# Kernel optimization log

Measured on AMD Instinct MI355X. Metric: run time of the kernel, lower is better.

Reference implementation:

```python
import jax, jax.numpy as jnp
import numpy as np

N_NODES = 50000
N_EDGES = 800000
F_IN = 128          # num_node_features == conv_size
L = 4               # num_conv_layers
LIN = 256
OUT = 10
N_GRAPHS = 64


def setup_inputs() -> dict:
    key = jax.random.key(0)
    ks = jax.random.split(key, 8)
    x = jax.random.normal(ks[0], (N_NODES, F_IN), dtype=jnp.float32)
    edge_index = jax.random.randint(ks[1], (2, N_EDGES), 0, N_NODES, dtype=jnp.int64)
    batch = jnp.sort(jax.random.randint(ks[2], (N_NODES,), 0, N_GRAPHS, dtype=jnp.int64))
    pos = jax.random.normal(ks[3], (N_NODES, 3), dtype=jnp.float32)
    # learned params: 4 GCN layers (all [F_IN,F_IN] since in==out==128), cat-JK head
    Ws = jax.random.normal(ks[4], (L, F_IN, F_IN), dtype=jnp.float32) * 0.05
    bs = jnp.zeros((L, F_IN), dtype=jnp.float32)
    Wlin = jax.random.normal(ks[5], (L * F_IN, LIN), dtype=jnp.float32) * 0.05
    blin = jnp.zeros((LIN,), dtype=jnp.float32)
    Wout = jax.random.normal(ks[6], (LIN, OUT), dtype=jnp.float32) * 0.05
    bout = jnp.zeros((OUT,), dtype=jnp.float32)
    return {"x": x, "edge_index": edge_index, "batch": batch, "pos": pos,
            "Ws": Ws, "bs": bs, "Wlin": Wlin, "blin": blin,
            "Wout": Wout, "bout": bout}


def reference(x, edge_index, batch, pos, Ws, bs, Wlin, blin, Wout, bout):
    N = x.shape[0]
    # GCN normalization with added self-loops (PyG gcn_norm, edge_weight=1)
    loop = jnp.arange(N, dtype=edge_index.dtype)
    src = jnp.concatenate([edge_index[0], loop])
    dst = jnp.concatenate([edge_index[1], loop])
    deg = jax.ops.segment_sum(jnp.ones_like(dst, dtype=x.dtype), dst, num_segments=N)
    dinv = jax.lax.rsqrt(deg)  # deg >= 1 due to self-loops
    norm = (dinv[src] * dinv[dst])[:, None]  # [E+N, 1]

    h = x
    xs = []
    for l in range(L):
        t = h @ Ws[l]                                    # [N, F]
        agg = jax.ops.segment_sum(t[src] * norm, dst, num_segments=N)
        h = jax.nn.relu(agg + bs[l])                     # dropout is identity in eval
        xs.append(h)
    hcat = jnp.concatenate(xs, axis=-1)                  # JK 'cat' -> [N, L*F]
    g = jax.ops.segment_max(hcat, batch, num_segments=N_GRAPHS)  # global_max_pool
    return jax.nn.relu(g @ Wlin + blin) @ Wout + bout    # [N_GRAPHS, OUT]
```

## Files before the change

### kernel.cpp

```cpp
#include <hip/hip_runtime.h>
#include <stdint.h>

#define NN    50000
#define NE    800000
#define FD    128
#define NLAY  4
#define NLIN  256
#define NOUTF 10
#define NGR   64
#define NBKT  196
#define MAXB  8192
#define GEMMB 782
#define POOLB 512

typedef _Float16 half8  __attribute__((ext_vector_type(8)));
typedef _Float16 half4  __attribute__((ext_vector_type(4)));
typedef _Float16 half2t __attribute__((ext_vector_type(2)));
typedef float    f32x4  __attribute__((ext_vector_type(4)));

__device__ __forceinline__ int ld_idx(const void* p, int flag, long i){
    return flag ? (int)((const long long*)p)[i] : ((const int*)p)[i];
}

__global__ __launch_bounds__(256) void pre_k(const unsigned* __restrict__ eidx_u,
                                             const float* __restrict__ Ws,
                                             _Float16* __restrict__ WT,
                                             int* __restrict__ zbase, int zn, int zb,
                                             int* __restrict__ sent,
                                             float* __restrict__ scl,
                                             int* __restrict__ flag){
    __shared__ int any;
    const int b = blockIdx.x, tid = threadIdx.x;
    if (b < 256){
        int idx = b*256 + tid;
        int l = idx >> 14;
        int r = idx & 16383;
        int c = r >> 7, k = r & 127;
        WT[idx] = (_Float16)Ws[(l<<14) + (k<<7) + c];
    } else if (b < 256 + zb){
        int i = (b-256)*256 + tid;
        if (i < zn) zbase[i] = 0;
    } else if (b == 256 + zb){
        if (tid < FD/4) sent[tid] = 0;
        if (tid == 0) scl[NN] = 0.f;
    } else {
        if (tid == 0) any = 0;
        __syncthreads();
        if (eidx_u[2*tid + 1] != 0u) atomicOr(&any, 1);
        __syncthreads();
        if (tid == 0) *flag = (any == 0) ? 1 : 0;
    }
}

__global__ __launch_bounds__(1024) void binB_k(const void* __restrict__ eidx,
                                               const int* __restrict__ flag,
                                               int* __restrict__ bktCur,
                                               unsigned* __restrict__ binned){
    __shared__ int hist[NBKT];
    __shared__ int resv[NBKT];
    __shared__ int cur[NBKT];
    const int tid = threadIdx.x;
    const int f = *flag;
    if (tid < NBKT){ hist[tid] = 0; cur[tid] = 0; }
    __syncthreads();

    int bkt[4]; unsigned pk[4];
    #pragma unroll
    for (int u = 0; u < 4; ++u){
        long e = (long)blockIdx.x*4096 + u*1024 + tid;
        if (e < NE){
            int s = ld_idx(eidx, f, e);
            int d = ld_idx(eidx, f, (long)NE + e);
            bkt[u] = d >> 8;
            pk[u]  = ((unsigned)(d & 255) << 16) | (unsigned)s;
            atomicAdd(&hist[bkt[u]], 1);
        } else bkt[u] = -1;
    }
    __syncthreads();
    if (tid < NBKT && hist[tid] > 0)
        resv[tid] = atomicAdd(&bktCur[tid], hist[tid]);
    __syncthreads();
    #pragma unroll
    for (int u = 0; u < 4; ++u){
        if (bkt[u] >= 0){
            int p = resv[bkt[u]] + atomicAdd(&cur[bkt[u]], 1);
            if ((unsigned)p < MAXB) binned[(long)bkt[u]*MAXB + p] = pk[u];
        }
    }
}

__global__ __launch_bounds__(256) void passC_k(const int* __restrict__ bktCur,
                                               const unsigned* __restrict__ binned,
                                               int* __restrict__ rp, int* __restrict__ re,
                                               float* __restrict__ dinv,
                                               unsigned short* __restrict__ cn,
                                               const void* __restrict__ batv,
                                               const int* __restrict__ flag,
                                               int* __restrict__ gstart){
    __shared__ unsigned staged[MAXB];
    __shared__ int cnt[256];
    __shared__ int sc[256];
    __shared__ int cur[256];
    const int tid = threadIdx.x;
    if (blockIdx.x >= NBKT){
        int i = (blockIdx.x - NBKT)*256 + tid;
        if (i >= NN) return;
        int f = *flag;
        int b = ld_idx(batv, f, i);
        if (i == 0){
            for (int g = 0; g <= b; ++g) gstart[g] = 0;
        } else {
            int p = ld_idx(batv, f, i-1);
            for (int g = p+1; g <= b; ++g) gstart[g] = i;
        }
        if (i == NN-1){
            for (int g = b+1; g <= NGR; ++g) gstart[g] = NN;
        }
        return;
    }
    const int b = blockIdx.x;
    int n = bktCur[b]; if (n > MAXB) n = MAXB;
    const long base = (long)b*MAXB;

    cnt[tid] = 0;
    __syncthreads();
    for (int i = tid; i < n; i += 256){
        unsigned rec = binned[base + i];
        staged[i] = rec;
        atomicAdd(&cnt[rec >> 16], 1);
    }
    __syncthreads();
    int c  = cnt[tid];
    int pc = (c + 15) & ~15;
    sc[tid] = pc;
    __syncthreads();
    for (int off = 1; off < 256; off <<= 1){
        int t = (tid >= off) ? sc[tid - off] : 0;
        __syncthreads();
        if (tid >= off) sc[tid] += t;
        __syncthreads();
    }
    int lo = sc[tid] - pc;
    int v = b*256 + tid;
    if (v < NN){
        rp[v]   = (int)base + lo;
        re[v]   = (int)base + lo + pc;
        dinv[v] = rsqrtf((float)(c + 1));
    }
    cur[tid] = lo;
    __syncthreads();
    for (int i = tid; i < n; i += 256){
        unsigned rec = staged[i];
        int j = rec >> 16;
        int p = atomicAdd(&cur[j], 1);
        cn[base + p] = (unsigned short)(rec & 0xFFFFu);
    }
    __syncthreads();
    for (int i = c; i < pc; ++i)
        cn[base + lo + i] = (unsigned short)NN;
}

template<bool F32IN, bool POOL>
__global__ __launch_bounds__(256) void gemm_k(const void* __restrict__ Av,
                                              const _Float16* __restrict__ WT,
                                              const float* __restrict__ dinv,
                                              unsigned char* __restrict__ T,
                                              float* __restrict__ scl,
                                              const _Float16* __restrict__ h,
                                              const int* __restrict__ gstart,
                                              unsigned* __restrict__ gbuf, int lpool){
    const int tid  = threadIdx.x;
    if (POOL && blockIdx.x >= GEMMB){
        __shared__ float red[4][FD];
        int pid = blockIdx.x - GEMMB;
        int g = pid >> 3, part = pid & 7;
        int lane = tid & 63, w = tid >> 6;
        int s0 = gstart[g], s1 = gstart[g+1];
        int len = s1 - s0;
        int chunk = (len + 7) >> 3;
        int a = s0 + part*chunk;
        int b = min(a + chunk, s1);
        int sub = (b - a + 3) >> 2;
        int aa = a + w*sub;
        int bb = min(aa + sub, b);
        const half2t* h2 = reinterpret_cast<const half2t*>(h);
        float m0 = 0.f, m1 = 0.f;
        for (int i = aa; i < bb; ++i){
            half2t x = h2[(long)i*64 + lane];
            m0 = fmaxf(m0, (float)x[0]);
            m1 = fmaxf(m1, (float)x[1]);
        }
        red[w][2*lane]   = m0;
        red[w][2*lane+1] = m1;
        __syncthreads();
        if (w == 0){
            float r0 = fmaxf(fmaxf(red[0][2*lane],   red[1][2*lane]),
                             fmaxf(red[2][2*lane],   red[3][2*lane]));
            float r1 = fmaxf(fmaxf(red[0][2*lane+1], red[1][2*lane+1]),
                             fmaxf(red[2][2*lane+1], red[3][2*lane+1]));
            atomicMax(&gbuf[g*(NLAY*FD) + lpool*FD + 2*lane    ], __float_as_uint(r0));
            atomicMax(&gbuf[g*(NLAY*FD) + lpool*FD + 2*lane + 1], __float_as_uint(r1));
        }
        return;
    }

    __shared__ unsigned char Asb[64*256];
    __shared__ float hm[64][2];
    const int lane = tid & 63;
    const int wid  = tid >> 6;
    const int wr   = (wid >> 1) * 32;
    const int wc   = (wid & 1) * 64;
    const long r0  = (long)blockIdx.x * 64;
    const int lr   = lane & 15;
    const int lk   = (lane >> 4) * 8;

    {
        int tr = tid >> 2, ch = tid & 3;
        long grow = r0 + tr;
        bool ok = grow < NN;
        #pragma unroll
        for (int i = 0; i < 4; ++i){
            half8 a;
            if constexpr (F32IN){
                const float* A = (const float*)Av;
                if (ok){
                    float4 u0 = *reinterpret_cast<const float4*>(A + grow*FD + ch*32 + i*8);
                    float4 u1 = *reinterpret_cast<const float4*>(A + grow*FD + ch*32 + i*8 + 4);
                    a[0]=(_Float16)u0.x; a[1]=(_Float16)u0.y; a[2]=(_Float16)u0.z; a[3]=(_Float16)u0.w;
                    a[4]=(_Float16)u1.x; a[5]=(_Float16)u1.y; a[6]=(_Float16)u1.z; a[7]=(_Float16)u1.w;
                } else a = (half8)(_Float16)0;
            } else {
                const _Float16* A = (const _Float16*)Av;
                a = ok ? *reinterpret_cast<const half8*>(A + grow*FD + ch*32 + i*8)
                       : (half8)(_Float16)0;
            }
            int off = (tr*256 + ch*64 + i*16) ^ ((tr & 7) << 4);
            *reinterpret_cast<half8*>(Asb + off) = a;
        }
    }

    half8 wf[4][4];
    #pragma unroll
    for (int n = 0; n < 4; ++n)
        #pragma unroll
        for (int kk = 0; kk < 4; ++kk)
            wf[n][kk] = *reinterpret_cast<const half8*>(WT + (wc + n*16 + lr)*FD + kk*32 + lk);

    f32x4 acc[2][4];
    #pragma unroll
    for (int m = 0; m < 2; ++m)
        #pragma unroll
        for (int n = 0; n < 4; ++n)
            acc[m][n] = (f32x4){0.f,0.f,0.f,0.f};

    __syncthreads();

    #pragma unroll
    for (int kk = 0; kk < 4; ++kk){
        half8 af[2];
        #pragma unroll
        for (int m = 0; m < 2; ++m){
            int rl = wr + m*16 + lr;
            int off = (rl*256 + kk*64 + (lane>>4)*16) ^ ((rl & 7) << 4);
            af[m] = *reinterpret_cast<const half8*>(Asb + off);
        }
        #pragma unroll
        for (int m = 0; m < 2; ++m)
            #pragma unroll
            for (int n = 0; n < 4; ++n)
                acc[m][n] = __builtin_amdgcn_mfma_f32_16x16x32_f16(wf[n][kk], af[m], acc[m][n], 0, 0, 0);
    }

    float amax[2] = {0.f, 0.f};
    float dim[2];
    #pragma unroll
    for (int m = 0; m < 2; ++m){
        long row = r0 + wr + m*16 + lr;
        float di = (row < NN) ? dinv[row] : 0.f;
        dim[m] = di;
        #pragma unroll
        for (int n = 0; n < 4; ++n)
            #pragma unroll
            for (int q = 0; q < 4; ++q)
                amax[m] = fmaxf(amax[m], fabsf(acc[m][n][q] * di));
    }
    #pragma unroll
    for (int m = 0; m < 2; ++m){
        amax[m] = fmaxf(amax[m], __shfl_xor(amax[m], 16));
        amax[m] = fmaxf(amax[m], __shfl_xor(amax[m], 32));
    }
    __syncthreads();
    if (lane < 16){
        hm[wr + lane     ][wid & 1] = amax[0];
        hm[wr + 16 + lane][wid & 1] = amax[1];
    }
    __syncthreads();
    #pragma unroll
    for (int m = 0; m < 2; ++m){
        long row = r0 + wr + m*16 + lr;
        if (row >= NN) continue;
        int rl = wr + m*16 + lr;
        float rm = fmaxf(hm[rl][0], hm[rl][1]);
        float a = rm * (1.0f/127.0f);
        unsigned bits = __float_as_uint(a);
        unsigned e = bits >> 23;
        unsigned sb = ((bits & 0x7fffffu) ? e + 1u : e) << 23;
        float scale = __uint_as_float(sb);
        float inv = __uint_as_float((254u - (sb >> 23)) << 23);
        if (rm < 1e-30f){ scale = 0.f; inv = 0.f; }
        float di = dim[m];
        #pragma unroll
        for (int n = 0; n < 4; ++n){
            int q0 = __float2int_rn(acc[m][n][0] * di * inv) + 128;
            int q1 = __float2int_rn(acc[m][n][1] * di * inv) + 128;
            int q2 = __float2int_rn(acc[m][n][2] * di * inv) + 128;
            int q3 = __float2int_rn(acc[m][n][3] * di * inv) + 128;
            unsigned p = (unsigned)q0 | ((unsigned)q1 << 8) |
                         ((unsigned)q2 << 16) | ((unsigned)q3 << 24);
            *reinterpret_cast<unsigned*>(T + (size_t)row*FD + wc + n*16 + (lane>>4)*4) = p;
        }
        if ((wid & 1) == 0 && lane < 16)
            scl[row] = scale;
    }
}

__global__ __launch_bounds__(256) void agg_k(const unsigned char* __restrict__ t,
                                             const float* __restrict__ scl,
                                             const int* __restrict__ rp,
                                             const int* __restrict__ re,
                                             const unsigned short* __restrict__ cn,
                                             const float* __restrict__ dinv,
                                             const float* __restrict__ bias,
                                             _Float16* __restrict__ h){
    const int lane = threadIdx.x & 63;
    const int wid  = threadIdx.x >> 6;
    const int r    = lane & 15;
    const int qb   = lane & 48;
    const int v    = blockIdx.x*16 + wid*4 + (lane >> 4);
    const uint2* tq = reinterpret_cast<const uint2*>(t);

    float acc[8];
    #pragma unroll
    for (int i = 0; i < 8; ++i) acc[i] = 0.f;
    float ssum = 0.f;

    const int e0 = rp[v], e1 = re[v];
    for (int base = e0; base < e1; base += 16){
        int ce = (int)cn[base + r];
        float scv = scl[ce];
        #pragma unroll
        for (int j = 0; j < 16; ++j){
            int s    = __shfl(ce,  qb + j);
            float sc = __shfl(scv, qb + j);
            uint2 g = tq[(size_t)s*16 + r];
            acc[0] = fmaf((float)( g.x        & 255u), sc, acc[0]);
            acc[1] = fmaf((float)((g.x >>  8) & 255u), sc, acc[1]);
            acc[2] = fmaf((float)((g.x >> 16) & 255u), sc, acc[2]);
            acc[3] = fmaf((float)( g.x >> 24        ), sc, acc[3]);
            acc[4] = fmaf((float)( g.y        & 255u), sc, acc[4]);
            acc[5] = fmaf((float)((g.y >>  8) & 255u), sc, acc[5]);
            acc[6] = fmaf((float)((g.y >> 16) & 255u), sc, acc[6]);
            acc[7] = fmaf((float)( g.y >> 24        ), sc, acc[7]);
            ssum += sc;
        }
    }
    {
        float sc = scl[v];
        uint2 g = tq[(size_t)v*16 + r];
        acc[0] = fmaf((float)( g.x        & 255u), sc, acc[0]);
        acc[1] = fmaf((float)((g.x >>  8) & 255u), sc, acc[1]);
        acc[2] = fmaf((float)((g.x >> 16) & 255u), sc, acc[2]);
        acc[3] = fmaf((float)( g.x >> 24        ), sc, acc[3]);
        acc[4] = fmaf((float)( g.y        & 255u), sc, acc[4]);
        acc[5] = fmaf((float)((g.y >>  8) & 255u), sc, acc[5]);
        acc[6] = fmaf((float)((g.y >> 16) & 255u), sc, acc[6]);
        acc[7] = fmaf((float)( g.y >> 24        ), sc, acc[7]);
        ssum += sc;
    }

    float dis = dinv[v];
    float4 b0 = reinterpret_cast<const float4*>(bias)[2*r];
    float4 b1 = reinterpret_cast<const float4*>(bias)[2*r+1];
    float bb[8] = {b0.x,b0.y,b0.z,b0.w,b1.x,b1.y,b1.z,b1.w};
    half8 o;
    #pragma unroll
    for (int i = 0; i < 8; ++i)
        o[i] = (_Float16)fmaxf(fmaf(acc[i] - 128.f*ssum, dis, bb[i]), 0.f);
    reinterpret_cast<half8*>(h)[(size_t)v*16 + r] = o;
}

__global__ __launch_bounds__(256) void pool_k(const _Float16* __restrict__ h,
                                              const int* __restrict__ gstart,
                                              unsigned* __restrict__ gbuf, int l){
    __shared__ float red[4][FD];
    int g = blockIdx.x, part = blockIdx.y;
    int tid = threadIdx.x, lane = tid & 63, w = tid >> 6;
    int s0 = gstart[g], s1 = gstart[g+1];
    int len = s1 - s0;
    int chunk = (len + 7) >> 3;
    int a = s0 + part*chunk;
    int b = min(a + chunk, s1);
    int sub = (b - a + 3) >> 2;
    int aa = a + w*sub;
    int bb = min(aa + sub, b);
    const half2t* h2 = reinterpret_cast<const half2t*>(h);
    float m0 = 0.f, m1 = 0.f;
    for (int i = aa; i < bb; ++i){
        half2t x = h2[(long)i*64 + lane];
        m0 = fmaxf(m0, (float)x[0]);
        m1 = fmaxf(m1, (float)x[1]);
    }
    red[w][2*lane]   = m0;
    red[w][2*lane+1] = m1;
    __syncthreads();
    if (w == 0){
        float r0 = fmaxf(fmaxf(red[0][2*lane],   red[1][2*lane]),
                         fmaxf(red[2][2*lane],   red[3][2*lane]));
        float r1 = fmaxf(fmaxf(red[0][2*lane+1], red[1][2*lane+1]),
                         fmaxf(red[2][2*lane+1], red[3][2*lane+1]));
        atomicMax(&gbuf[g*(NLAY*FD) + l*FD + 2*lane    ], __float_as_uint(r0));
        atomicMax(&gbuf[g*(NLAY*FD) + l*FD + 2*lane + 1], __float_as_uint(r1));
    }
}

__global__ __launch_bounds__(1024) void head_k(const unsigned* __restrict__ gbuf,
                                               const float* __restrict__ Wlin,
                                               const float* __restrict__ blin,
                                               const float* __restrict__ Wout,
                                               const float* __restrict__ bout,
                                               float* __restrict__ out){
    __shared__ float gs[NLAY*FD];
    __shared__ float ps[4][NLIN];
    __shared__ float us[NLIN];
    int g = blockIdx.x, tid = threadIdx.x;
    if (tid < NLAY*FD) gs[tid] = __uint_as_float(gbuf[g*(NLAY*FD) + tid]);
    __syncthreads();
    int c = tid & 255;
    int q = tid >> 8;
    float a = 0.f;
    #pragma unroll 8
    for (int k = q*128; k < q*128 + 128; ++k)
        a = fmaf(gs[k], Wlin[k*NLIN + c], a);
    ps[q][c] = a;
    __syncthreads();
    if (tid < NLIN){
        float u = ps[0][tid] + ps[1][tid] + ps[2][tid] + ps[3][tid] + blin[tid];
        us[tid] = fmaxf(u, 0.f);
    }
    __syncthreads();
    if (tid < NOUTF){
        float o = bout[tid];
        #pragma unroll 8
        for (int k = 0; k < NLIN; ++k) o = fmaf(us[k], Wout[k*NOUTF + tid], o);
        out[g*NOUTF + tid] = o;
    }
}

extern "C" void kernel_launch(void* const* d_in, const int* in_sizes, int n_in,
                              void* d_out, int out_size, void* d_ws, size_t ws_size,
                              hipStream_t stream){
    const float* x    = (const float*)d_in[0];
    const void*  eidx = d_in[1];
    const void*  batv = d_in[2];
    const float* Wsp  = (const float*)d_in[4];
    const float* bsp  = (const float*)d_in[5];
    const float* Wlin = (const float*)d_in[6];
    const float* blin = (const float*)d_in[7];
    const float* Wout = (const float*)d_in[8];
    const float* bout = (const float*)d_in[9];
    float* out = (float*)d_out;

    uintptr_t cur = (uintptr_t)d_ws;
    auto alloc = [&](size_t bytes)->void*{
        cur = (cur + 255) & ~(uintptr_t)255;
        void* p = (void*)cur;
        cur += bytes;
        return p;
    };
    unsigned char* t = (unsigned char*)alloc((size_t)(NN+1)*FD);
    float* scl   = (float*)alloc((size_t)(NN+1)*4);
    _Float16* h  = (_Float16*)alloc((size_t)NN*FD*2);
    _Float16* WT = (_Float16*)alloc((size_t)NLAY*FD*FD*2);
    unsigned* binned = (unsigned*)alloc((size_t)NBKT*MAXB*4);
    unsigned short* cn = (unsigned short*)alloc((size_t)NBKT*MAXB*2);
    int*   rp    = (int*)  alloc((size_t)NN*4);
    int*   re    = (int*)  alloc((size_t)NN*4);
    float* dinv  = (float*)alloc((size_t)NN*4);
    int*   gst   = (int*)  alloc((NGR+1)*4);
    int*   flag  = (int*)  alloc(4);
    int*      bktCur = (int*)     alloc((size_t)NBKT*4);
    unsigned* gbuf   = (unsigned*)alloc((size_t)NGR*NLAY*FD*4);
    int zero_n = (int)((cur - (uintptr_t)bktCur + 3) / 4);
    int zb = (zero_n + 255) / 256;

    pre_k  <<<256 + zb + 2, 256, 0, stream>>>((const unsigned*)eidx, Wsp, WT,
                                              bktCur, zero_n, zb,
                                              (int*)(t + (size_t)NN*FD), scl, flag);
    binB_k <<<NBKT, 1024, 0, stream>>>(eidx, flag, bktCur, binned);
    passC_k<<<NBKT + (NN+255)/256, 256, 0, stream>>>(bktCur, binned, rp, re, dinv, cn,
                                                     batv, flag, gst);

    for (int l = 0; l < NLAY; ++l){
        const void* hin = (l == 0) ? (const void*)x : (const void*)h;
        if (l == 0)
            gemm_k<true ,false><<<GEMMB, 256, 0, stream>>>(hin, WT, dinv, t, scl,
                                                           h, gst, gbuf, 0);
        else
            gemm_k<false,true ><<<GEMMB + POOLB, 256, 0, stream>>>(hin, WT + (size_t)l*FD*FD,
                                                                   dinv, t, scl, h, gst, gbuf, l-1);
        agg_k<<<NN/16, 256, 0, stream>>>(t, scl, rp, re, cn, dinv, bsp + (size_t)l*FD, h);
    }
    pool_k<<<dim3(NGR, 8), 256, 0, stream>>>(h, gst, gbuf, NLAY-1);
    head_k<<<NGR, 1024, 0, stream>>>(gbuf, Wlin, blin, Wout, bout, out);
}
```

Measured before the change: 229.4 us.

## Split int8 feature table into two 64-column planes for half-width gather

The quantized feature table is stored as two separate planes of 64 columns each, and the aggregation kernel runs twice as many blocks. Each block handles one half of the feature columns, and block indices are interleaved so both halves of neighbouring node groups run close together. The aim is a smaller per-plane working set that fits the cache better during the random neighbour gather, plus more parallelism. It also switches the GEMM and aggregation output writes to nontemporal stores. The cost is that neighbour indices and scales are loaded twice, and each gather moves only 4 bytes per lane.

```diff
diff --git a/kernel.cpp b/kernel.cpp
--- a/kernel.cpp
+++ b/kernel.cpp
@@ -12,6 +12,8 @@
 #define MAXB  8192
 #define GEMMB 782
 #define POOLB 512
+#define PLSZ  ((size_t)(NN+1)*64)
+#define AGGB  6256
 
 typedef _Float16 half8  __attribute__((ext_vector_type(8)));
 typedef _Float16 half4  __attribute__((ext_vector_type(4)));
@@ -26,7 +28,7 @@
                                              const float* __restrict__ Ws,
                                              _Float16* __restrict__ WT,
                                              int* __restrict__ zbase, int zn, int zb,
-                                             int* __restrict__ sent,
+                                             unsigned char* __restrict__ t,
                                              float* __restrict__ scl,
                                              int* __restrict__ flag){
     __shared__ int any;
@@ -41,7 +43,8 @@
         int i = (b-256)*256 + tid;
         if (i < zn) zbase[i] = 0;
     } else if (b == 256 + zb){
-        if (tid < FD/4) sent[tid] = 0;
+        if (tid < 16) ((int*)(t + (size_t)NN*64))[tid] = 0;
+        else if (tid < 32) ((int*)(t + PLSZ + (size_t)NN*64))[tid-16] = 0;
         if (tid == 0) scl[NN] = 0.f;
     } else {
         if (tid == 0) any = 0;
@@ -295,6 +298,7 @@
         hm[wr + 16 + lane][wid & 1] = amax[1];
     }
     __syncthreads();
+    unsigned char* Tp = T + (size_t)(wc >> 6) * PLSZ;
     #pragma unroll
     for (int m = 0; m < 2; ++m){
         long row = r0 + wr + m*16 + lr;
@@ -317,7 +321,8 @@
             int q3 = __float2int_rn(acc[m][n][3] * di * inv) + 128;
             unsigned p = (unsigned)q0 | ((unsigned)q1 << 8) |
                          ((unsigned)q2 << 16) | ((unsigned)q3 << 24);
-            *reinterpret_cast<unsigned*>(T + (size_t)row*FD + wc + n*16 + (lane>>4)*4) = p;
+            __builtin_nontemporal_store(p,
+                reinterpret_cast<unsigned*>(Tp + (size_t)row*64 + n*16 + (lane>>4)*4));
         }
         if ((wid & 1) == 0 && lane < 16)
             scl[row] = scale;
@@ -332,16 +337,19 @@
                                              const float* __restrict__ dinv,
                                              const float* __restrict__ bias,
                                              _Float16* __restrict__ h){
+    const int bid = blockIdx.x;
+    const int x   = bid & 7;
+    const int fh  = x >> 2;
+    const int nb  = (bid >> 3)*4 + (x & 3);
+    if (nb >= NN/16) return;
     const int lane = threadIdx.x & 63;
     const int wid  = threadIdx.x >> 6;
     const int r    = lane & 15;
     const int qb   = lane & 48;
-    const int v    = blockIdx.x*16 + wid*4 + (lane >> 4);
-    const uint2* tq = reinterpret_cast<const uint2*>(t);
-
-    float acc[8];
-    #pragma unroll
-    for (int i = 0; i < 8; ++i) acc[i] = 0.f;
+    const int v    = nb*16 + wid*4 + (lane >> 4);
+    const unsigned* plane = reinterpret_cast<const unsigned*>(t + (size_t)fh * PLSZ);
+
+    float acc[4] = {0.f, 0.f, 0.f, 0.f};
     float ssum = 0.f;
 
     const int e0 = rp[v], e1 = re[v];
@@ -352,41 +360,35 @@
         for (int j = 0; j < 16; ++j){
             int s    = __shfl(ce,  qb + j);
             float sc = __shfl(scv, qb + j);
-            uint2 g = tq[(size_t)s*16 + r];
-            acc[0] = fmaf((float)( g.x        & 255u), sc, acc[0]);
-            acc[1] = fmaf((float)((g.x >>  8) & 255u), sc, acc[1]);
-            acc[2] = fmaf((float)((g.x >> 16) & 255u), sc, acc[2]);
-            acc[3] = fmaf((float)( g.x >> 24        ), sc, acc[3]);
-            acc[4] = fmaf((float)( g.y        & 255u), sc, acc[4]);
-            acc[5] = fmaf((float)((g.y >>  8) & 255u), sc, acc[5]);
-            acc[6] = fmaf((float)((g.y >> 16) & 255u), sc, acc[6]);
-            acc[7] = fmaf((float)( g.y >> 24        ), sc, acc[7]);
+            unsigned g = plane[(size_t)s*16 + r];
+            acc[0] = fmaf((float)( g        & 255u), sc, acc[0]);
+            acc[1] = fmaf((float)((g >>  8) & 255u), sc, acc[1]);
+            acc[2] = fmaf((float)((g >> 16) & 255u), sc, acc[2]);
+            acc[3] = fmaf((float)( g >> 24        ), sc, acc[3]);
             ssum += sc;
         }
     }
     {
         float sc = scl[v];
-        uint2 g = tq[(size_t)v*16 + r];
-        acc[0] = fmaf((float)( g.x        & 255u), sc, acc[0]);
-        acc[1] = fmaf((float)((g.x >>  8) & 255u), sc, acc[1]);
-        acc[2] = fmaf((float)((g.x >> 16) & 255u), sc, acc[2]);
-        acc[3] = fmaf((float)( g.x >> 24        ), sc, acc[3]);
-        acc[4] = fmaf((float)( g.y        & 255u), sc, acc[4]);
-        acc[5] = fmaf((float)((g.y >>  8) & 255u), sc, acc[5]);
-        acc[6] = fmaf((float)((g.y >> 16) & 255u), sc, acc[6]);
-        acc[7] = fmaf((float)( g.y >> 24        ), sc, acc[7]);
+        unsigned g = plane[(size_t)v*16 + r];
+        acc[0] = fmaf((float)( g        & 255u), sc, acc[0]);
+        acc[1] = fmaf((float)((g >>  8) & 255u), sc, acc[1]);
+        acc[2] = fmaf((float)((g >> 16) & 255u), sc, acc[2]);
+        acc[3] = fmaf((float)( g >> 24        ), sc, acc[3]);
         ssum += sc;
     }
 
     float dis = dinv[v];
-    float4 b0 = reinterpret_cast<const float4*>(bias)[2*r];
-    float4 b1 = reinterpret_cast<const float4*>(bias)[2*r+1];
-    float bb[8] = {b0.x,b0.y,b0.z,b0.w,b1.x,b1.y,b1.z,b1.w};
-    half8 o;
-    #pragma unroll
-    for (int i = 0; i < 8; ++i)
+    float4 b = reinterpret_cast<const float4*>(bias)[fh*16 + r];
+    float bb[4] = {b.x, b.y, b.z, b.w};
+    half4 o;
+    #pragma unroll
+    for (int i = 0; i < 4; ++i)
         o[i] = (_Float16)fmaxf(fmaf(acc[i] - 128.f*ssum, dis, bb[i]), 0.f);
-    reinterpret_cast<half8*>(h)[(size_t)v*16 + r] = o;
+    unsigned long long uu;
+    __builtin_memcpy(&uu, &o, 8);
+    __builtin_nontemporal_store(uu,
+        reinterpret_cast<unsigned long long*>(h + (size_t)v*FD + fh*64 + r*4));
 }
 
 __global__ __launch_bounds__(256) void pool_k(const _Float16* __restrict__ h,
@@ -477,7 +479,7 @@
         cur += bytes;
         return p;
     };
-    unsigned char* t = (unsigned char*)alloc((size_t)(NN+1)*FD);
+    unsigned char* t = (unsigned char*)alloc(2*PLSZ);
     float* scl   = (float*)alloc((size_t)(NN+1)*4);
     _Float16* h  = (_Float16*)alloc((size_t)NN*FD*2);
     _Float16* WT = (_Float16*)alloc((size_t)NLAY*FD*FD*2);
@@ -494,8 +496,7 @@
     int zb = (zero_n + 255) / 256;
 
     pre_k  <<<256 + zb + 2, 256, 0, stream>>>((const unsigned*)eidx, Wsp, WT,
-                                              bktCur, zero_n, zb,
-                                              (int*)(t + (size_t)NN*FD), scl, flag);
+                                              bktCur, zero_n, zb, t, scl, flag);
     binB_k <<<NBKT, 1024, 0, stream>>>(eidx, flag, bktCur, binned);
     passC_k<<<NBKT + (NN+255)/256, 256, 0, stream>>>(bktCur, binned, rp, re, dinv, cn,
                                                      batv, flag, gst);
@@ -508,7 +509,7 @@
         else
             gemm_k<false,true ><<<GEMMB + POOLB, 256, 0, stream>>>(hin, WT + (size_t)l*FD*FD,
                                                                    dinv, t, scl, h, gst, gbuf, l-1);
-        agg_k<<<NN/16, 256, 0, stream>>>(t, scl, rp, re, cn, dinv, bsp + (size_t)l*FD, h);
+        agg_k<<<AGGB, 256, 0, stream>>>(t, scl, rp, re, cn, dinv, bsp + (size_t)l*FD, h);
     }
     pool_k<<<dim3(NGR, 8), 256, 0, stream>>>(h, gst, gbuf, NLAY-1);
     head_k<<<NGR, 1024, 0, stream>>>(gbuf, Wlin, blin, Wout, bout, out);
```

Measured after the change: 235.7 us. 2.7% more time.
